# Performance work log

Measured on AMD Instinct MI355X. Metric: run time of the kernel, lower is better.

Reference implementation:

```python
import jax, jax.numpy as jnp
import numpy as np

N = 100000      # nodes
E = 1_600_000   # edges (avg degree 16)
DIMS = [(64, 64), (64, 64), (64, 40)]  # gnn_layers [64,64,64,40]


def setup_inputs() -> dict:
    key = jax.random.key(0)
    ks = jax.random.split(key, 2 + 3 * len(DIMS))
    inp = {
        "x": jax.random.normal(ks[0], (N, DIMS[0][0]), jnp.float32),
        "edge_index": jax.random.randint(ks[1], (2, E), 0, N),
    }
    k = 2
    for i, (din, dout) in enumerate(DIMS):
        s = 1.0 / np.sqrt(din)
        inp[f"Wl{i}"] = jax.random.uniform(ks[k], (din, dout), jnp.float32, -s, s); k += 1
        inp[f"bl{i}"] = jax.random.uniform(ks[k], (dout,), jnp.float32, -s, s); k += 1
        inp[f"Wr{i}"] = jax.random.uniform(ks[k], (din, dout), jnp.float32, -s, s); k += 1
    return inp


def _sage_conv(x, src, dst, Wl, bl, Wr):
    # PyG SAGEConv (mean aggr): out = lin_l(mean_{j in N(i)} x_j) + lin_r(x_i)
    deg = jax.ops.segment_sum(jnp.ones((src.shape[0],), x.dtype), dst, num_segments=N)
    agg = jax.ops.segment_sum(x[src], dst, num_segments=N)  # [N, din] scatter-add
    agg = agg / jnp.clip(deg, 1.0)[:, None]                  # mean; isolated nodes -> 0
    return agg @ Wl + bl + x @ Wr


def reference(x, edge_index, Wl0, bl0, Wr0, Wl1, bl1, Wr1, Wl2, bl2, Wr2):
    src, dst = edge_index[0], edge_index[1]
    h = x
    params = [(Wl0, bl0, Wr0), (Wl1, bl1, Wr1), (Wl2, bl2, Wr2)]
    for i, (Wl, bl, Wr) in enumerate(params):
        h = _sage_conv(h, src, dst, Wl, bl, Wr)
        if i != len(params) - 1:
            h = jax.nn.relu(h)
            # F.dropout with training=False is identity (eval mode)
    return jax.nn.log_softmax(h, axis=1)
```

## Files before the change

kernel.cpp:

```cpp
#include <hip/hip_runtime.h>
#include <math.h>

#define ACT_RELU 0
#define ACT_LSM  1
#define BSH 8
#define MAXNB 512

typedef __attribute__((ext_vector_type(8))) short bf16x8;
typedef __attribute__((ext_vector_type(4))) float f32x4;

__device__ __forceinline__ unsigned f2bf(float f) {
  unsigned u = __float_as_uint(f);
  u += 0x7fffu + ((u >> 16) & 1u);
  return u >> 16;
}
__device__ __forceinline__ float bflo(unsigned u) { return __uint_as_float(u << 16); }
__device__ __forceinline__ float bfhi(unsigned u) { return __uint_as_float(u & 0xffff0000u); }

__global__ void k_zero(int* __restrict__ p, int n) {
  int i = blockIdx.x * 256 + threadIdx.x;
  if (i < n) p[i] = 0;
}

__global__ void k_histB(const int* __restrict__ dst, int* __restrict__ bucket_cnt,
                        int E, int NB) {
  __shared__ int cntL[MAXNB];
  int t = threadIdx.x;
  for (int b = t; b < NB; b += 256) cntL[b] = 0;
  __syncthreads();
  int e0 = blockIdx.x * 4096;
  int e1 = min(e0 + 4096, E);
  for (int i = e0 + t; i < e1; i += 256) atomicAdd(&cntL[dst[i] >> BSH], 1);
  __syncthreads();
  for (int b = t; b < NB; b += 256)
    if (cntL[b]) atomicAdd(&bucket_cnt[b], cntL[b]);
}

__global__ void k_bscan(const int* __restrict__ bucket_cnt, int* __restrict__ bucket_base,
                        int* __restrict__ bucket_cursor, int NB) {
  __shared__ int sm[MAXNB];
  int t = threadIdx.x;
  sm[t] = (t < NB) ? bucket_cnt[t] : 0;
  __syncthreads();
  for (int off = 1; off < MAXNB; off <<= 1) {
    int x = (t >= off) ? sm[t - off] : 0;
    __syncthreads();
    sm[t] += x;
    __syncthreads();
  }
  int ex = (t == 0) ? 0 : sm[t - 1];
  if (t <= NB) bucket_base[t] = ex;
  if (t < NB) bucket_cursor[t] = ex;
}

__global__ void k_partition(const int* __restrict__ src, const int* __restrict__ dst,
                            int* __restrict__ bucket_cursor, int2* __restrict__ tmp,
                            int E, int NB) {
  __shared__ int cntL[MAXNB];
  __shared__ int baseL[MAXNB];
  int t = threadIdx.x;
  for (int b = t; b < NB; b += 256) cntL[b] = 0;
  __syncthreads();
  int e0 = blockIdx.x * 4096;
  int e1 = min(e0 + 4096, E);
  for (int i = e0 + t; i < e1; i += 256) atomicAdd(&cntL[dst[i] >> BSH], 1);
  __syncthreads();
  for (int b = t; b < NB; b += 256) {
    int c = cntL[b];
    baseL[b] = c ? atomicAdd(&bucket_cursor[b], c) : 0;
    cntL[b] = 0;
  }
  __syncthreads();
  for (int i = e0 + t; i < e1; i += 256) {
    int s = src[i], d = dst[i];
    int b = d >> BSH;
    int r = atomicAdd(&cntL[b], 1);
    tmp[baseL[b] + r] = make_int2(s, d);
  }
}

__global__ void __launch_bounds__(256) k_bmake(const int2* __restrict__ tmp,
                                               const int* __restrict__ bucket_base,
                                               int* __restrict__ row_ptr,
                                               int* __restrict__ edge_src,
                                               int N, int E, int NB) {
  __shared__ int cntL[256];
  __shared__ int scanL[256];
  int b = blockIdx.x;
  int t = threadIdx.x;
  int e0 = bucket_base[b], e1 = bucket_base[b + 1];
  cntL[t] = 0;
  __syncthreads();
  for (int i = e0 + t; i < e1; i += 256) atomicAdd(&cntL[tmp[i].y & 255], 1);
  __syncthreads();
  int v = cntL[t];
  scanL[t] = v;
  __syncthreads();
  for (int off = 1; off < 256; off <<= 1) {
    int x = (t >= off) ? scanL[t - off] : 0;
    __syncthreads();
    scanL[t] += x;
    __syncthreads();
  }
  int exc = scanL[t] - v;
  int node = (b << BSH) + t;
  if (node < N) row_ptr[node] = e0 + exc;
  if (b == NB - 1 && t == 0) row_ptr[N] = E;
  __syncthreads();
  cntL[t] = e0 + exc;
  __syncthreads();
  for (int i = e0 + t; i < e1; i += 256) {
    int2 e = tmp[i];
    int p = atomicAdd(&cntL[e.y & 255], 1);
    edge_src[p] = e.x;
  }
}

__global__ void k_hist(const int* __restrict__ dst, int* __restrict__ cnt, int E) {
  int i = blockIdx.x * blockDim.x + threadIdx.x;
  if (i < E) atomicAdd(&cnt[dst[i]], 1);
}

__global__ void k_scan_part(const int* __restrict__ cnt, int* __restrict__ bsum, int M) {
  __shared__ int sm[256];
  int t = threadIdx.x;
  int base = blockIdx.x * 2048 + t * 8;
  int s = 0;
#pragma unroll
  for (int j = 0; j < 8; ++j) { int i = base + j; if (i < M) s += cnt[i]; }
  sm[t] = s;
  __syncthreads();
  for (int off = 128; off > 0; off >>= 1) {
    if (t < off) sm[t] += sm[t + off];
    __syncthreads();
  }
  if (t == 0) bsum[blockIdx.x] = sm[0];
}

__global__ void k_scan_mid(const int* __restrict__ bsum, int* __restrict__ boff, int nb) {
  int l = threadIdx.x;
  int v = (l < nb) ? bsum[l] : 0;
  int inc = v;
  for (int off = 1; off < 64; off <<= 1) {
    int u = __shfl_up(inc, off);
    if (l >= off) inc += u;
  }
  if (l < nb) boff[l] = inc - v;
}

__global__ void k_scan_final(const int* __restrict__ cnt, const int* __restrict__ boff,
                             int* __restrict__ row_ptr, int* __restrict__ cursor, int M) {
  __shared__ int sm[256];
  int t = threadIdx.x;
  int base = blockIdx.x * 2048 + t * 8;
  int v[8];
  int s = 0;
#pragma unroll
  for (int j = 0; j < 8; ++j) { int i = base + j; v[j] = (i < M) ? cnt[i] : 0; s += v[j]; }
  sm[t] = s;
  __syncthreads();
  for (int off = 1; off < 256; off <<= 1) {
    int x = (t >= off) ? sm[t - off] : 0;
    __syncthreads();
    sm[t] += x;
    __syncthreads();
  }
  int run = boff[blockIdx.x] + sm[t] - s;
#pragma unroll
  for (int j = 0; j < 8; ++j) {
    int i = base + j;
    if (i < M) { row_ptr[i] = run; cursor[i] = run; }
    run += v[j];
  }
}

__global__ void k_fill(const int* __restrict__ src, const int* __restrict__ dst,
                       int* __restrict__ cursor, int* __restrict__ edge_src, int E) {
  int i = blockIdx.x * blockDim.x + threadIdx.x;
  if (i < E) {
    int d = dst[i];
    int p = atomicAdd(&cursor[d], 1);
    edge_src[p] = src[i];
  }
}

__global__ void __launch_bounds__(256) k_cast(const float* __restrict__ x,
                                              unsigned short* __restrict__ xb, int n) {
  int i = blockIdx.x * 256 + threadIdx.x;
  if (i * 8 < n) {
    const float4* p = (const float4*)(x + (size_t)i * 8);
    float4 a = p[0], b = p[1];
    uint4 w;
    w.x = f2bf(a.x) | (f2bf(a.y) << 16);
    w.y = f2bf(a.z) | (f2bf(a.w) << 16);
    w.z = f2bf(b.x) | (f2bf(b.y) << 16);
    w.w = f2bf(b.z) | (f2bf(b.w) << 16);
    *(uint4*)(xb + (size_t)i * 8) = w;
  }
}

template <int DOUT, int ACT>
__global__ void __launch_bounds__(256) k_layer(const unsigned short* __restrict__ h,
                                               const int* __restrict__ row_ptr,
                                               const int* __restrict__ edge_src,
                                               const float* __restrict__ Wl,
                                               const float* __restrict__ Wr,
                                               const float* __restrict__ bias,
                                               void* __restrict__ outv, int n) {
  constexpr int NT = (DOUT + 15) / 16;
  constexpr int PADN = NT * 16;
  __shared__ unsigned short Wlds[128 * PADN];
  __shared__ unsigned short meanL[4][16 * 72];
  int t = threadIdx.x;

  for (int idx = t; idx < 128 * PADN; idx += 256) {
    int k = idx / PADN, nn = idx % PADN;
    float v = 0.f;
    if (nn < DOUT) v = (k < 64) ? Wl[k * DOUT + nn] : Wr[(k - 64) * DOUT + nn];
    int fi = ((((k >> 5) * NT + (nn >> 4)) * 16 + (nn & 15)) * 4 + ((k >> 3) & 3)) * 8 + (k & 7);
    Wlds[fi] = (unsigned short)f2bf(v);
  }

  int w = t >> 6, lane = t & 63;
  int r0 = (blockIdx.x * 4 + w) * 16;
  int g = lane & 7;

  for (int half = 0; half < 2; ++half) {
    int node = half * 8 + (lane >> 3);
    int i = r0 + node;
    float a[8];
#pragma unroll
    for (int c = 0; c < 8; ++c) a[c] = 0.f;
    float scale = 0.f;
    if (i < n) {
      int rp0 = row_ptr[i], rp1 = row_ptr[i + 1];
      int deg = rp1 - rp0;
      scale = (deg > 0) ? (1.0f / (float)deg) : 0.f;
      for (int base = 0; base < deg; base += 8) {
        int idx = rp0 + base + g;
        int sv = (idx < rp1) ? edge_src[idx] : 0;
        int cnt = min(8, deg - base);
        uint4 v0, v1, v2, v3, v4, v5, v6, v7;
#pragma unroll
        for (int e = 0; e < 8; ++e) {
          int s = __shfl(sv, (lane & ~7) | e);
          const uint4* p = (const uint4*)(h + (size_t)s * 64) + g;
          if (e == 0 && e < cnt) v0 = *p;
          if (e == 1 && e < cnt) v1 = *p;
          if (e == 2 && e < cnt) v2 = *p;
          if (e == 3 && e < cnt) v3 = *p;
          if (e == 4 && e < cnt) v4 = *p;
          if (e == 5 && e < cnt) v5 = *p;
          if (e == 6 && e < cnt) v6 = *p;
          if (e == 7 && e < cnt) v7 = *p;
        }
#define ACCUM(vv, ee)                                                   \
        if ((ee) < cnt) {                                               \
          a[0] += bflo(vv.x); a[1] += bfhi(vv.x);                       \
          a[2] += bflo(vv.y); a[3] += bfhi(vv.y);                       \
          a[4] += bflo(vv.z); a[5] += bfhi(vv.z);                       \
          a[6] += bflo(vv.w); a[7] += bfhi(vv.w);                       \
        }
        ACCUM(v0, 0) ACCUM(v1, 1) ACCUM(v2, 2) ACCUM(v3, 3)
        ACCUM(v4, 4) ACCUM(v5, 5) ACCUM(v6, 6) ACCUM(v7, 7)
#undef ACCUM
      }
    }
    uint4 wv;
    wv.x = f2bf(a[0] * scale) | (f2bf(a[1] * scale) << 16);
    wv.y = f2bf(a[2] * scale) | (f2bf(a[3] * scale) << 16);
    wv.z = f2bf(a[4] * scale) | (f2bf(a[5] * scale) << 16);
    wv.w = f2bf(a[6] * scale) | (f2bf(a[7] * scale) << 16);
    *(uint4*)&meanL[w][node * 72 + g * 8] = wv;
  }
  __syncthreads();

  int c = lane & 15;
  int kb = lane >> 4;
  bf16x8 bf[4][NT];
#pragma unroll
  for (int s = 0; s < 4; ++s)
#pragma unroll
    for (int nt = 0; nt < NT; ++nt)
      bf[s][nt] = *(const bf16x8*)&Wlds[(((s * NT + nt) * 16 + c) * 4 + kb) * 8];

  bf16x8 af[4];
  af[0] = *(const bf16x8*)&meanL[w][c * 72 + kb * 8];
  af[1] = *(const bf16x8*)&meanL[w][c * 72 + 32 + kb * 8];
  int row = r0 + c;
  if (row >= n) row = n - 1;
  size_t rb = (size_t)row * 64 + kb * 8;
  af[2] = *(const bf16x8*)(h + rb);
  af[3] = *(const bf16x8*)(h + rb + 32);

  f32x4 acc[NT];
#pragma unroll
  for (int nt = 0; nt < NT; ++nt) acc[nt] = (f32x4){0.f, 0.f, 0.f, 0.f};
#pragma unroll
  for (int s = 0; s < 4; ++s)
#pragma unroll
    for (int nt = 0; nt < NT; ++nt)
      acc[nt] = __builtin_amdgcn_mfma_f32_16x16x32_bf16(af[s], bf[s][nt], acc[nt], 0, 0, 0);

  int rbase = r0 + kb * 4;
  if (ACT == ACT_RELU) {
    unsigned short* out = (unsigned short*)outv;
#pragma unroll
    for (int nt = 0; nt < NT; ++nt) {
      float bval = bias[nt * 16 + c];
#pragma unroll
      for (int r = 0; r < 4; ++r) {
        int R = rbase + r;
        if (R < n) {
          float v = fmaxf(acc[nt][r] + bval, 0.f);
          out[(size_t)R * DOUT + nt * 16 + c] = (unsigned short)f2bf(v);
        }
      }
    }
  } else {
    float* out = (float*)outv;
    float bv[NT];
#pragma unroll
    for (int nt = 0; nt < NT; ++nt) bv[nt] = ((nt * 16 + c) < DOUT) ? bias[nt * 16 + c] : 0.f;
#pragma unroll
    for (int r = 0; r < 4; ++r) {
      int R = rbase + r;
      float v[NT];
      float m = -INFINITY;
#pragma unroll
      for (int nt = 0; nt < NT; ++nt) {
        bool valid = (nt * 16 + c) < DOUT;
        v[nt] = valid ? (acc[nt][r] + bv[nt]) : -INFINITY;
        m = fmaxf(m, v[nt]);
      }
#pragma unroll
      for (int off = 1; off < 16; off <<= 1) m = fmaxf(m, __shfl_xor(m, off));
      float es = 0.f;
#pragma unroll
      for (int nt = 0; nt < NT; ++nt)
        if ((nt * 16 + c) < DOUT) es += expf(v[nt] - m);
#pragma unroll
      for (int off = 1; off < 16; off <<= 1) es += __shfl_xor(es, off);
      float lse = logf(es);
      if (R < n) {
#pragma unroll
        for (int nt = 0; nt < NT; ++nt)
          if ((nt * 16 + c) < DOUT) out[(size_t)R * DOUT + nt * 16 + c] = v[nt] - m - lse;
      }
    }
  }
}

extern "C" void kernel_launch(void* const* d_in, const int* in_sizes, int n_in,
                              void* d_out, int out_size, void* d_ws, size_t ws_size,
                              hipStream_t stream) {
  const float* x   = (const float*)d_in[0];
  const int*   ei  = (const int*)d_in[1];
  const float* Wl0 = (const float*)d_in[2];
  const float* bl0 = (const float*)d_in[3];
  const float* Wr0 = (const float*)d_in[4];
  const float* Wl1 = (const float*)d_in[5];
  const float* bl1 = (const float*)d_in[6];
  const float* Wr1 = (const float*)d_in[7];
  const float* Wl2 = (const float*)d_in[8];
  const float* bl2 = (const float*)d_in[9];
  const float* Wr2 = (const float*)d_in[10];
  float* out = (float*)d_out;

  int N = in_sizes[0] / 64;
  int E = in_sizes[1] / 2;
  int M = N + 1;
  int NB = (N + 255) >> BSH;
  const int* src = ei;
  const int* dst = ei + E;

  char* p = (char*)d_ws;
  auto alloc = [&](size_t bytes) {
    char* r = p;
    p += (bytes + 255) & ~(size_t)255;
    return r;
  };
  int* cnt      = (int*)alloc((size_t)M * 4);
  int* row_ptr  = (int*)alloc((size_t)M * 4);
  int* cursor   = (int*)alloc((size_t)M * 4);
  int* bsum     = (int*)alloc(256 * 4);
  int* boff     = (int*)alloc(256 * 4);
  int* bk_cnt   = (int*)alloc((MAXNB + 1) * 4);
  int* bk_base  = (int*)alloc((MAXNB + 1) * 4);
  int* bk_cur   = (int*)alloc((MAXNB + 1) * 4);
  int* edge_src = (int*)alloc((size_t)E * 4);
  size_t szR1 = (size_t)E * 8 > (size_t)N * 128 ? (size_t)E * 8 : (size_t)N * 128;
  char* R1            = alloc(szR1);
  unsigned short* hbA = (unsigned short*)alloc((size_t)N * 128);
  unsigned short* hbB = (unsigned short*)alloc((size_t)N * 128);
  if ((size_t)(p - (char*)d_ws) > ws_size) return;

  bool bucketed = (NB <= MAXNB);
  int eb4 = (E + 4095) / 4096;

  if (bucketed) {
    k_zero<<<(MAXNB + 256) / 256, 256, 0, stream>>>(bk_cnt, MAXNB + 1);
    k_histB<<<eb4, 256, 0, stream>>>(dst, bk_cnt, E, NB);
    k_bscan<<<1, MAXNB, 0, stream>>>(bk_cnt, bk_base, bk_cur, NB);
    k_partition<<<eb4, 256, 0, stream>>>(src, dst, bk_cur, (int2*)R1, E, NB);
    k_bmake<<<NB, 256, 0, stream>>>((const int2*)R1, bk_base, row_ptr, edge_src, N, E, NB);
  } else {
    k_zero<<<(M + 255) / 256, 256, 0, stream>>>(cnt, M);
    k_hist<<<(E + 255) / 256, 256, 0, stream>>>(dst, cnt, E);
    int nb = (M + 2047) / 2048;
    k_scan_part<<<nb, 256, 0, stream>>>(cnt, bsum, M);
    k_scan_mid<<<1, 64, 0, stream>>>(bsum, boff, nb);
    k_scan_final<<<nb, 256, 0, stream>>>(cnt, boff, row_ptr, cursor, M);
    k_fill<<<(E + 255) / 256, 256, 0, stream>>>(src, dst, cursor, edge_src, E);
  }

  unsigned short* xb = (unsigned short*)R1;

  int cb = (N * 64 / 8 + 255) / 256;
  int gb = (N + 63) / 64;

  k_cast<<<cb, 256, 0, stream>>>(x, xb, N * 64);
  k_layer<64, ACT_RELU><<<gb, 256, 0, stream>>>(xb, row_ptr, edge_src, Wl0, Wr0, bl0, hbA, N);
  k_layer<64, ACT_RELU><<<gb, 256, 0, stream>>>(hbA, row_ptr, edge_src, Wl1, Wr1, bl1, hbB, N);
  k_layer<40, ACT_LSM><<<gb, 256, 0, stream>>>(hbB, row_ptr, edge_src, Wl2, Wr2, bl2, out, N);
}
```

Before: 208.8 us.

## Gather neighbor features in FP8 copies to halve aggregation traffic

Each layer now writes an extra FP8 copy of its activations, and the input cast produces one too. The neighbor gather reads these 8-byte FP8 rows instead of 16-byte bf16 rows and converts them with packed fp8-to-f32 instructions. The self term and the matmul still use bf16. The aim is to cut the bandwidth of the random-access gather, which is the dominant cost, at the price of extra byte stores and a loss of precision in the mean aggregation. The LDS padding and weight-staging index math are also changed, and buffers are reused to make room.

```diff
diff --git a/kernel.cpp b/kernel.cpp
--- a/kernel.cpp
+++ b/kernel.cpp
@@ -8,14 +8,20 @@
 
 typedef __attribute__((ext_vector_type(8))) short bf16x8;
 typedef __attribute__((ext_vector_type(4))) float f32x4;
+typedef __attribute__((ext_vector_type(2))) float f32x2;
 
 __device__ __forceinline__ unsigned f2bf(float f) {
   unsigned u = __float_as_uint(f);
   u += 0x7fffu + ((u >> 16) & 1u);
   return u >> 16;
 }
-__device__ __forceinline__ float bflo(unsigned u) { return __uint_as_float(u << 16); }
-__device__ __forceinline__ float bfhi(unsigned u) { return __uint_as_float(u & 0xffff0000u); }
+template <bool HI>
+__device__ __forceinline__ f32x2 f8cvt(unsigned w) {
+  return __builtin_amdgcn_cvt_pk_f32_fp8((int)w, HI);
+}
+__device__ __forceinline__ unsigned char f2f8(float v) {
+  return (unsigned char)(__builtin_amdgcn_cvt_pk_fp8_f32(v, v, 0, false) & 0xff);
+}
 
 __global__ void k_zero(int* __restrict__ p, int n) {
   int i = blockIdx.x * 256 + threadIdx.x;
@@ -185,7 +191,8 @@
 }
 
 __global__ void __launch_bounds__(256) k_cast(const float* __restrict__ x,
-                                              unsigned short* __restrict__ xb, int n) {
+                                              unsigned short* __restrict__ xb,
+                                              unsigned char* __restrict__ x8, int n) {
   int i = blockIdx.x * 256 + threadIdx.x;
   if (i * 8 < n) {
     const float4* p = (const float4*)(x + (size_t)i * 8);
@@ -196,34 +203,51 @@
     w.z = f2bf(b.x) | (f2bf(b.y) << 16);
     w.w = f2bf(b.z) | (f2bf(b.w) << 16);
     *(uint4*)(xb + (size_t)i * 8) = w;
-  }
-}
+    uint2 q;
+    q.x = (unsigned)__builtin_amdgcn_cvt_pk_fp8_f32(a.x, a.y, 0, false);
+    q.x = (unsigned)__builtin_amdgcn_cvt_pk_fp8_f32(a.z, a.w, (int)q.x, true);
+    q.y = (unsigned)__builtin_amdgcn_cvt_pk_fp8_f32(b.x, b.y, 0, false);
+    q.y = (unsigned)__builtin_amdgcn_cvt_pk_fp8_f32(b.z, b.w, (int)q.y, true);
+    *(uint2*)(x8 + (size_t)i * 8) = q;
+  }
+}
+
+#define MPAD 80
 
 template <int DOUT, int ACT>
 __global__ void __launch_bounds__(256) k_layer(const unsigned short* __restrict__ h,
+                                               const unsigned char* __restrict__ h8,
                                                const int* __restrict__ row_ptr,
                                                const int* __restrict__ edge_src,
                                                const float* __restrict__ Wl,
                                                const float* __restrict__ Wr,
                                                const float* __restrict__ bias,
-                                               void* __restrict__ outv, int n) {
+                                               void* __restrict__ outv,
+                                               unsigned char* __restrict__ out8, int n) {
   constexpr int NT = (DOUT + 15) / 16;
   constexpr int PADN = NT * 16;
   __shared__ unsigned short Wlds[128 * PADN];
-  __shared__ unsigned short meanL[4][16 * 72];
-  int t = threadIdx.x;
-
-  for (int idx = t; idx < 128 * PADN; idx += 256) {
-    int k = idx / PADN, nn = idx % PADN;
+  __shared__ unsigned short meanL[4][16 * MPAD];
+  int t = threadIdx.x;
+
+  for (int fi = t; fi < 128 * PADN; fi += 256) {
+    int k7 = fi & 7;
+    int kb = (fi >> 3) & 3;
+    int c16 = (fi >> 5) & 15;
+    int rest = fi >> 9;
+    int nt = rest % NT;
+    int kb5 = rest / NT;
+    int k = kb5 * 32 + kb * 8 + k7;
+    int nn = nt * 16 + c16;
     float v = 0.f;
     if (nn < DOUT) v = (k < 64) ? Wl[k * DOUT + nn] : Wr[(k - 64) * DOUT + nn];
-    int fi = ((((k >> 5) * NT + (nn >> 4)) * 16 + (nn & 15)) * 4 + ((k >> 3) & 3)) * 8 + (k & 7);
     Wlds[fi] = (unsigned short)f2bf(v);
   }
 
   int w = t >> 6, lane = t & 63;
   int r0 = (blockIdx.x * 4 + w) * 16;
   int g = lane & 7;
+  int lb = lane & ~7;
 
   for (int half = 0; half < 2; ++half) {
     int node = half * 8 + (lane >> 3);
@@ -240,11 +264,11 @@
         int idx = rp0 + base + g;
         int sv = (idx < rp1) ? edge_src[idx] : 0;
         int cnt = min(8, deg - base);
-        uint4 v0, v1, v2, v3, v4, v5, v6, v7;
+        uint2 v0, v1, v2, v3, v4, v5, v6, v7;
 #pragma unroll
         for (int e = 0; e < 8; ++e) {
-          int s = __shfl(sv, (lane & ~7) | e);
-          const uint4* p = (const uint4*)(h + (size_t)s * 64) + g;
+          int s = __shfl(sv, lb | e);
+          const uint2* p = (const uint2*)(h8 + (size_t)s * 64) + g;
           if (e == 0 && e < cnt) v0 = *p;
           if (e == 1 && e < cnt) v1 = *p;
           if (e == 2 && e < cnt) v2 = *p;
@@ -254,12 +278,12 @@
           if (e == 6 && e < cnt) v6 = *p;
           if (e == 7 && e < cnt) v7 = *p;
         }
-#define ACCUM(vv, ee)                                                   \
-        if ((ee) < cnt) {                                               \
-          a[0] += bflo(vv.x); a[1] += bfhi(vv.x);                       \
-          a[2] += bflo(vv.y); a[3] += bfhi(vv.y);                       \
-          a[4] += bflo(vv.z); a[5] += bfhi(vv.z);                       \
-          a[6] += bflo(vv.w); a[7] += bfhi(vv.w);                       \
+#define ACCUM(vv, ee)                                                    \
+        if ((ee) < cnt) {                                                \
+          f32x2 p0 = f8cvt<false>(vv.x), p1 = f8cvt<true>(vv.x);         \
+          f32x2 p2 = f8cvt<false>(vv.y), p3 = f8cvt<true>(vv.y);         \
+          a[0] += p0.x; a[1] += p0.y; a[2] += p1.x; a[3] += p1.y;        \
+          a[4] += p2.x; a[5] += p2.y; a[6] += p3.x; a[7] += p3.y;        \
         }
         ACCUM(v0, 0) ACCUM(v1, 1) ACCUM(v2, 2) ACCUM(v3, 3)
         ACCUM(v4, 4) ACCUM(v5, 5) ACCUM(v6, 6) ACCUM(v7, 7)
@@ -271,7 +295,7 @@
     wv.y = f2bf(a[2] * scale) | (f2bf(a[3] * scale) << 16);
     wv.z = f2bf(a[4] * scale) | (f2bf(a[5] * scale) << 16);
     wv.w = f2bf(a[6] * scale) | (f2bf(a[7] * scale) << 16);
-    *(uint4*)&meanL[w][node * 72 + g * 8] = wv;
+    *(uint4*)&meanL[w][node * MPAD + g * 8] = wv;
   }
   __syncthreads();
 
@@ -285,8 +309,8 @@
       bf[s][nt] = *(const bf16x8*)&Wlds[(((s * NT + nt) * 16 + c) * 4 + kb) * 8];
 
   bf16x8 af[4];
-  af[0] = *(const bf16x8*)&meanL[w][c * 72 + kb * 8];
-  af[1] = *(const bf16x8*)&meanL[w][c * 72 + 32 + kb * 8];
+  af[0] = *(const bf16x8*)&meanL[w][c * MPAD + kb * 8];
+  af[1] = *(const bf16x8*)&meanL[w][c * MPAD + 32 + kb * 8];
   int row = r0 + c;
   if (row >= n) row = n - 1;
   size_t rb = (size_t)row * 64 + kb * 8;
@@ -313,7 +337,9 @@
         int R = rbase + r;
         if (R < n) {
           float v = fmaxf(acc[nt][r] + bval, 0.f);
-          out[(size_t)R * DOUT + nt * 16 + c] = (unsigned short)f2bf(v);
+          size_t o = (size_t)R * DOUT + nt * 16 + c;
+          out[o] = (unsigned short)f2bf(v);
+          out8[o] = f2f8(v);
         }
       }
     }
@@ -390,9 +416,10 @@
   int* bk_cur   = (int*)alloc((MAXNB + 1) * 4);
   int* edge_src = (int*)alloc((size_t)E * 4);
   size_t szR1 = (size_t)E * 8 > (size_t)N * 128 ? (size_t)E * 8 : (size_t)N * 128;
-  char* R1            = alloc(szR1);
-  unsigned short* hbA = (unsigned short*)alloc((size_t)N * 128);
-  unsigned short* hbB = (unsigned short*)alloc((size_t)N * 128);
+  char* R1              = alloc(szR1);
+  unsigned short* hbA   = (unsigned short*)alloc((size_t)N * 128);
+  unsigned char*  P8A   = (unsigned char*)alloc((size_t)N * 64);
+  unsigned char*  P8B   = (unsigned char*)alloc((size_t)N * 64);
   if ((size_t)(p - (char*)d_ws) > ws_size) return;
 
   bool bucketed = (NB <= MAXNB);
@@ -414,13 +441,17 @@
     k_fill<<<(E + 255) / 256, 256, 0, stream>>>(src, dst, cursor, edge_src, E);
   }
 
-  unsigned short* xb = (unsigned short*)R1;
+  unsigned short* xb  = (unsigned short*)R1;
+  unsigned short* hbB = (unsigned short*)R1;
+  unsigned char*  x8  = P8A;
+  unsigned char*  h8A = P8B;
+  unsigned char*  h8B = P8A;
 
   int cb = (N * 64 / 8 + 255) / 256;
   int gb = (N + 63) / 64;
 
-  k_cast<<<cb, 256, 0, stream>>>(x, xb, N * 64);
-  k_layer<64, ACT_RELU><<<gb, 256, 0, stream>>>(xb, row_ptr, edge_src, Wl0, Wr0, bl0, hbA, N);
-  k_layer<64, ACT_RELU><<<gb, 256, 0, stream>>>(hbA, row_ptr, edge_src, Wl1, Wr1, bl1, hbB, N);
-  k_layer<40, ACT_LSM><<<gb, 256, 0, stream>>>(hbB, row_ptr, edge_src, Wl2, Wr2, bl2, out, N);
-}
+  k_cast<<<cb, 256, 0, stream>>>(x, xb, x8, N * 64);
+  k_layer<64, ACT_RELU><<<gb, 256, 0, stream>>>(xb, x8, row_ptr, edge_src, Wl0, Wr0, bl0, hbA, h8A, N);
+  k_layer<64, ACT_RELU><<<gb, 256, 0, stream>>>(hbA, h8A, row_ptr, edge_src, Wl1, Wr1, bl1, hbB, h8B, N);
+  k_layer<40, ACT_LSM><<<gb, 256, 0, stream>>>(hbB, h8B, row_ptr, edge_src, Wl2, Wr2, bl2, out, nullptr, N);
+}
```

New measurement: 221.8 us. 6.2% more time.

## Prepack bf16 weights once and drop per-block LDS weight staging

Applied to the files above, without the earlier changes.

Weight conversion and swizzling into the MFMA fragment layout moves out of every layer block into small k_prepw kernels that write bf16 weights to workspace. Layer blocks then read B fragments straight from global/L2 per k-step instead of staging them in LDS. This removes a block-wide __syncthreads (replaced by a wave-local fence, since meanL is per-wave) and cuts LDS use, which may raise occupancy. It also pads meanL rows to 80 and reuses the R1 buffer for hbB. The costs are three extra kernel launches and repeated global reads of the weights by every block.

```diff
diff --git a/kernel.cpp b/kernel.cpp
--- a/kernel.cpp
+++ b/kernel.cpp
@@ -5,6 +5,7 @@
 #define ACT_LSM  1
 #define BSH 8
 #define MAXNB 512
+#define MPAD 80
 
 typedef __attribute__((ext_vector_type(8))) short bf16x8;
 typedef __attribute__((ext_vector_type(4))) float f32x4;
@@ -199,28 +200,37 @@
   }
 }
 
+template <int DOUT>
+__global__ void k_prepw(const float* __restrict__ Wl, const float* __restrict__ Wr,
+                        unsigned short* __restrict__ Wb) {
+  constexpr int NT = (DOUT + 15) / 16;
+  constexpr int PADN = NT * 16;
+  int fi = blockIdx.x * 256 + threadIdx.x;
+  if (fi < 128 * PADN) {
+    int k7 = fi & 7;
+    int kb = (fi >> 3) & 3;
+    int c16 = (fi >> 5) & 15;
+    int rest = fi >> 9;
+    int nt = rest % NT;
+    int kb5 = rest / NT;
+    int k = kb5 * 32 + kb * 8 + k7;
+    int nn = nt * 16 + c16;
+    float v = 0.f;
+    if (nn < DOUT) v = (k < 64) ? Wl[k * DOUT + nn] : Wr[(k - 64) * DOUT + nn];
+    Wb[fi] = (unsigned short)f2bf(v);
+  }
+}
+
 template <int DOUT, int ACT>
 __global__ void __launch_bounds__(256) k_layer(const unsigned short* __restrict__ h,
                                                const int* __restrict__ row_ptr,
                                                const int* __restrict__ edge_src,
-                                               const float* __restrict__ Wl,
-                                               const float* __restrict__ Wr,
+                                               const unsigned short* __restrict__ Wb,
                                                const float* __restrict__ bias,
                                                void* __restrict__ outv, int n) {
   constexpr int NT = (DOUT + 15) / 16;
-  constexpr int PADN = NT * 16;
-  __shared__ unsigned short Wlds[128 * PADN];
-  __shared__ unsigned short meanL[4][16 * 72];
-  int t = threadIdx.x;
-
-  for (int idx = t; idx < 128 * PADN; idx += 256) {
-    int k = idx / PADN, nn = idx % PADN;
-    float v = 0.f;
-    if (nn < DOUT) v = (k < 64) ? Wl[k * DOUT + nn] : Wr[(k - 64) * DOUT + nn];
-    int fi = ((((k >> 5) * NT + (nn >> 4)) * 16 + (nn & 15)) * 4 + ((k >> 3) & 3)) * 8 + (k & 7);
-    Wlds[fi] = (unsigned short)f2bf(v);
-  }
-
+  __shared__ unsigned short meanL[4][16 * MPAD];
+  int t = threadIdx.x;
   int w = t >> 6, lane = t & 63;
   int r0 = (blockIdx.x * 4 + w) * 16;
   int g = lane & 7;
@@ -271,22 +281,15 @@
     wv.y = f2bf(a[2] * scale) | (f2bf(a[3] * scale) << 16);
     wv.z = f2bf(a[4] * scale) | (f2bf(a[5] * scale) << 16);
     wv.w = f2bf(a[6] * scale) | (f2bf(a[7] * scale) << 16);
-    *(uint4*)&meanL[w][node * 72 + g * 8] = wv;
-  }
-  __syncthreads();
+    *(uint4*)&meanL[w][node * MPAD + g * 8] = wv;
+  }
+  __threadfence_block();
 
   int c = lane & 15;
   int kb = lane >> 4;
-  bf16x8 bf[4][NT];
-#pragma unroll
-  for (int s = 0; s < 4; ++s)
-#pragma unroll
-    for (int nt = 0; nt < NT; ++nt)
-      bf[s][nt] = *(const bf16x8*)&Wlds[(((s * NT + nt) * 16 + c) * 4 + kb) * 8];
-
   bf16x8 af[4];
-  af[0] = *(const bf16x8*)&meanL[w][c * 72 + kb * 8];
-  af[1] = *(const bf16x8*)&meanL[w][c * 72 + 32 + kb * 8];
+  af[0] = *(const bf16x8*)&meanL[w][c * MPAD + kb * 8];
+  af[1] = *(const bf16x8*)&meanL[w][c * MPAD + 32 + kb * 8];
   int row = r0 + c;
   if (row >= n) row = n - 1;
   size_t rb = (size_t)row * 64 + kb * 8;
@@ -297,10 +300,15 @@
 #pragma unroll
   for (int nt = 0; nt < NT; ++nt) acc[nt] = (f32x4){0.f, 0.f, 0.f, 0.f};
 #pragma unroll
-  for (int s = 0; s < 4; ++s)
+  for (int s = 0; s < 4; ++s) {
+    bf16x8 bft[NT];
 #pragma unroll
     for (int nt = 0; nt < NT; ++nt)
-      acc[nt] = __builtin_amdgcn_mfma_f32_16x16x32_bf16(af[s], bf[s][nt], acc[nt], 0, 0, 0);
+      bft[nt] = *(const bf16x8*)&Wb[(((s * NT + nt) * 16 + c) * 4 + kb) * 8];
+#pragma unroll
+    for (int nt = 0; nt < NT; ++nt)
+      acc[nt] = __builtin_amdgcn_mfma_f32_16x16x32_bf16(af[s], bft[nt], acc[nt], 0, 0, 0);
+  }
 
   int rbase = r0 + kb * 4;
   if (ACT == ACT_RELU) {
@@ -390,13 +398,19 @@
   int* bk_cur   = (int*)alloc((MAXNB + 1) * 4);
   int* edge_src = (int*)alloc((size_t)E * 4);
   size_t szR1 = (size_t)E * 8 > (size_t)N * 128 ? (size_t)E * 8 : (size_t)N * 128;
-  char* R1            = alloc(szR1);
-  unsigned short* hbA = (unsigned short*)alloc((size_t)N * 128);
-  unsigned short* hbB = (unsigned short*)alloc((size_t)N * 128);
+  char* R1              = alloc(szR1);
+  unsigned short* hbA   = (unsigned short*)alloc((size_t)N * 128);
+  unsigned short* Wb0   = (unsigned short*)alloc(128 * 64 * 2);
+  unsigned short* Wb1   = (unsigned short*)alloc(128 * 64 * 2);
+  unsigned short* Wb2   = (unsigned short*)alloc(128 * 48 * 2);
   if ((size_t)(p - (char*)d_ws) > ws_size) return;
 
   bool bucketed = (NB <= MAXNB);
   int eb4 = (E + 4095) / 4096;
+
+  k_prepw<64><<<(128 * 64 + 255) / 256, 256, 0, stream>>>(Wl0, Wr0, Wb0);
+  k_prepw<64><<<(128 * 64 + 255) / 256, 256, 0, stream>>>(Wl1, Wr1, Wb1);
+  k_prepw<40><<<(128 * 48 + 255) / 256, 256, 0, stream>>>(Wl2, Wr2, Wb2);
 
   if (bucketed) {
     k_zero<<<(MAXNB + 256) / 256, 256, 0, stream>>>(bk_cnt, MAXNB + 1);
@@ -414,13 +428,14 @@
     k_fill<<<(E + 255) / 256, 256, 0, stream>>>(src, dst, cursor, edge_src, E);
   }
 
-  unsigned short* xb = (unsigned short*)R1;
+  unsigned short* xb  = (unsigned short*)R1;
+  unsigned short* hbB = (unsigned short*)R1;
 
   int cb = (N * 64 / 8 + 255) / 256;
   int gb = (N + 63) / 64;
 
   k_cast<<<cb, 256, 0, stream>>>(x, xb, N * 64);
-  k_layer<64, ACT_RELU><<<gb, 256, 0, stream>>>(xb, row_ptr, edge_src, Wl0, Wr0, bl0, hbA, N);
-  k_layer<64, ACT_RELU><<<gb, 256, 0, stream>>>(hbA, row_ptr, edge_src, Wl1, Wr1, bl1, hbB, N);
-  k_layer<40, ACT_LSM><<<gb, 256, 0, stream>>>(hbB, row_ptr, edge_src, Wl2, Wr2, bl2, out, N);
-}
+  k_layer<64, ACT_RELU><<<gb, 256, 0, stream>>>(xb, row_ptr, edge_src, Wb0, bl0, hbA, N);
+  k_layer<64, ACT_RELU><<<gb, 256, 0, stream>>>(hbA, row_ptr, edge_src, Wb1, bl1, hbB, N);
+  k_layer<40, ACT_LSM><<<gb, 256, 0, stream>>>(hbB, row_ptr, edge_src, Wb2, bl2, out, N);
+}
```

Measured after the change: 196.2 us. 6.1% less time.
